# Optimization experiments

Hardware: AMD Instinct MI355X
Metric: run time of the kernel (lower is better)

## Reference

```python
import jax, jax.numpy as jnp
import numpy as np

T, N, F, L, A = 4, 16, 6, 1024, 21  # genomes, tiles, frames, tile length, alphabet
K, U = 20, 256                      # profile width, number of profiles


def setup_inputs() -> dict:
    key = jax.random.key(0)
    k1, k2 = jax.random.split(key)
    X = jax.random.uniform(k1, (T, N, F, L, A), dtype=jnp.float32)
    Q = jnp.ones((A,), dtype=jnp.float32) / A  # uniform background distribution
    # P_logit ~ log(Q) + N(0, 4) as in _getRandomProfiles
    P_logit = (jnp.log(Q)[None, :, None]
               + 4.0 * jax.random.normal(k2, (K, A, U), dtype=jnp.float32))
    return {"X": X, "P_logit": P_logit, "Q": Q}


def reference(X, P_logit, Q):
    # SpecificProfile.call(X) -> (S, R, Z)
    Tb, Nb, Fb, Lb, Ab = X.shape
    k, _, units = P_logit.shape
    # getR: P = softmax(P_logit, axis=1); R = log(max(P / Q, epsilon))
    P = jax.nn.softmax(P_logit, axis=1)                    # [k, A, U]
    epsilon = jnp.mean(Q)                                   # exp(-log(1/mean(Q)))
    R = jnp.log(jnp.maximum(P / Q[None, :, None], epsilon))  # [k, A, U]
    # getZ: conv2d over (length, alphabet) spatial dims, VALID padding
    Xr = X.reshape(Tb * Nb * Fb, Lb, Ab, 1)                 # NHWC
    Kr = R[:, :, None, :]                                   # HWIO: [k, A, 1, U]
    Z = jax.lax.conv_general_dilated(
        Xr, Kr, window_strides=(1, 1), padding='VALID',
        dimension_numbers=('NHWC', 'HWIO', 'NHWC'))          # [TNF, L-k+1, 1, U]
    Z = Z.reshape(Tb, Nb, Fb, Lb - k + 1, units)            # [T, N, F, P, U]
    S = jnp.max(Z, axis=(2, 3))                             # [T, N, U]
    return S, R, Z
```

## Files before the change

### kernel.cpp

```cpp
#include <hip/hip_runtime.h>
#include <hip/hip_bf16.h>
#include <math.h>

#define T_ 4
#define N_ 16
#define F_ 6
#define L_ 1024
#define A_ 21
#define K_ 20
#define U_ 256
#define LOUT 1005
#define NIMG 384
#define SZ_S (T_*N_*U_)
#define SZ_R (K_*A_*U_)

#define XPR 24
#define XROWS 1056
#define NSTEP 15
#define XWCH 7

typedef __attribute__((ext_vector_type(8))) short short8;
typedef __attribute__((ext_vector_type(4))) float f32x4;
typedef __attribute__((ext_vector_type(4))) unsigned int uint4v;

__device__ __forceinline__ unsigned short f2bf(float f) {
  unsigned int u = __float_as_uint(f);
  u += 0x7FFFu + ((u >> 16) & 1u);
  return (unsigned short)(u >> 16);
}

__device__ __forceinline__ void atomicMaxF(float* addr, float val) {
  if (val >= 0.f) atomicMax((int*)addr, __float_as_int(val));
  else            atomicMin((unsigned int*)addr, __float_as_uint(val));
}

__device__ __forceinline__ void gload_lds16(const void* g, void* l) {
  __builtin_amdgcn_global_load_lds(
      (const __attribute__((address_space(1))) void*)g,
      (__attribute__((address_space(3))) void*)l, 16, 0, 0);
}

__global__ void xprep_kernel(const float* __restrict__ X,
                             const float* __restrict__ P_logit,
                             const float* __restrict__ Q,
                             float* __restrict__ out,
                             unsigned short* __restrict__ Rt,
                             unsigned int* __restrict__ Xp32) {
  int t = blockIdx.x * blockDim.x + threadIdx.x;
  if (t < SZ_S) out[t] = -INFINITY;

  if (t < K_ * U_) {
    int k = t / U_;
    int u = t - k * U_;
    const float* pl = P_logit + (size_t)k * A_ * U_ + u;
    float v[A_];
    float m = -INFINITY;
#pragma unroll
    for (int a = 0; a < A_; ++a) { v[a] = pl[(size_t)a * U_]; m = fmaxf(m, v[a]); }
    float s = 0.f;
#pragma unroll
    for (int a = 0; a < A_; ++a) { v[a] = expf(v[a] - m); s += v[a]; }
    float qs = 0.f;
#pragma unroll
    for (int a = 0; a < A_; ++a) qs += Q[a];
    float eps = qs * (1.0f / A_);
    float invs = 1.f / s;
    float* Rout = out + SZ_S;
#pragma unroll
    for (int a = 0; a < XPR; ++a) {
      unsigned short bv = 0;
      if (a < A_) {
        float r = logf(fmaxf(v[a] * invs / Q[a], eps));
        Rout[(size_t)(k * A_ + a) * U_ + u] = r;
        bv = f2bf(r);
      }
      int sl = k * XPR + a;
      Rt[(size_t)(sl >> 5) * (U_ * 32) + u * 32 + (sl & 31)] = bv;
    }
  }

  if (t < NIMG * XROWS * 12) {
    int w  = t % 12;
    int rl = t / 12;
    int row = rl % XROWS;
    int n   = rl / XROWS;
    int c0 = w * 2;
    float v0 = 0.f, v1 = 0.f;
    if (row < L_) {
      const float* xr = X + ((size_t)n * L_ + row) * A_;
      if (c0 < A_)     v0 = xr[c0];
      if (c0 + 1 < A_) v1 = xr[c0 + 1];
    }
    unsigned int o = (unsigned int)f2bf(v0) | ((unsigned int)f2bf(v1) << 16);
    Xp32[(size_t)rl * 12 + w] = o;
  }
}

__global__ __launch_bounds__(256, 1) void conv_kernel(
    const unsigned short* __restrict__ Xp,
    const unsigned short* __restrict__ Rt,
    float* __restrict__ out) {
  __shared__ __align__(16) unsigned short lds_r[NSTEP * 4096];
  __shared__ __align__(16) unsigned short lds_xp[4][XWCH * 512];

  const int n  = blockIdx.z;
  const int u0 = blockIdx.x * 128;
  const int wid  = threadIdx.x >> 6;
  const int lane = threadIdx.x & 63;
  const int wl = wid >> 1;
  const int wu = wid & 1;

  const char* xsrc = (const char*)Xp +
      ((size_t)n * XROWS + wl * 128) * (XPR * 2);
  const char* rsrc = (const char*)Rt + (size_t)u0 * 64;
  char* xdst = (char*)&lds_xp[wid][0];

  for (int c = wid; c < NSTEP * 8; c += 4)
    gload_lds16(rsrc + (size_t)(c >> 3) * (U_ * 64) + (c & 7) * 1024 + lane * 16,
                (char*)lds_r + c * 1024);
#pragma unroll
  for (int c = 0; c < XWCH; ++c)
    gload_lds16(xsrc + c * 1024 + lane * 16, xdst + c * 1024);
  asm volatile("s_waitcnt vmcnt(0)" ::: "memory");
  __builtin_amdgcn_s_barrier();

  const int fl = lane & 15;
  const int fj = lane >> 4;
  const int rfo = (wu * 64 + fl) * 32 + (fj << 3);
  const unsigned short* xb =
      (const unsigned short*)xdst + fl * XPR + (fj << 3);
  const int ug = fj << 2;

  float* Z = out + SZ_S + SZ_R;
  float pmax[4][4];
#pragma unroll
  for (int ut = 0; ut < 4; ++ut)
#pragma unroll
    for (int r = 0; r < 4; ++r) pmax[ut][r] = -INFINITY;

  f32x4 accA[4][8], accB[4][8];
  uint4v xr[XWCH];

#define ZERO(ACC)                                                            \
  {                                                                          \
    _Pragma("unroll")                                                        \
    for (int ut = 0; ut < 4; ++ut)                                           \
      _Pragma("unroll")                                                      \
      for (int lt = 0; lt < 8; ++lt)                                         \
        (ACC)[ut][lt] = (f32x4){0.f, 0.f, 0.f, 0.f};                         \
  }

#define KSTEP(K, ACC)                                                        \
  {                                                                          \
    short8 xfr[8], rfr[4];                                                   \
    const unsigned short* rb = lds_r + (K) * 4096 + rfo;                     \
    _Pragma("unroll")                                                        \
    for (int lt = 0; lt < 8; ++lt)                                           \
      xfr[lt] = *(const short8*)(xb + lt * (16 * XPR) + (K) * 32);           \
    _Pragma("unroll")                                                        \
    for (int ut = 0; ut < 4; ++ut)                                           \
      rfr[ut] = *(const short8*)(rb + ut * (16 * 32));                       \
    _Pragma("unroll")                                                        \
    for (int ut = 0; ut < 4; ++ut)                                           \
      _Pragma("unroll")                                                      \
      for (int lt = 0; lt < 8; ++lt)                                         \
        (ACC)[ut][lt] = __builtin_amdgcn_mfma_f32_16x16x32_bf16(             \
            rfr[ut], xfr[lt], (ACC)[ut][lt], 0, 0, 0);                       \
  }

#define STORE4(ACC, TT, LT)                                                  \
  {                                                                          \
    const int l = (TT) * 256 + wl * 128 + (LT) * 16 + fl;                    \
    float* zrow = Z + ((size_t)n * LOUT + l) * U_ + u0 + wu * 64 + ug;       \
    _Pragma("unroll")                                                        \
    for (int ut = 0; ut < 4; ++ut) {                                         \
      f32x4 v = (ACC)[ut][LT];                                               \
      *(f32x4*)(zrow + ut * 16) = v;                                         \
      _Pragma("unroll")                                                      \
      for (int r = 0; r < 4; ++r) pmax[ut][r] = fmaxf(pmax[ut][r], v[r]);    \
    }                                                                        \
  }

#define XLOADS(T1)                                                           \
  {                                                                          \
    const char* xs = xsrc + (size_t)(T1) * (256 * XPR * 2);                  \
    _Pragma("unroll")                                                        \
    for (int c = 0; c < XWCH; ++c)                                           \
      xr[c] = *(const uint4v*)(xs + c * 1024 + lane * 16);                   \
  }

#define XWRITE()                                                             \
  {                                                                          \
    _Pragma("unroll")                                                        \
    for (int c = 0; c < XWCH; ++c)                                           \
      *(uint4v*)(xdst + c * 1024 + lane * 16) = xr[c];                       \
  }

  ZERO(accA)
  XLOADS(1)
#pragma unroll
  for (int k = 0; k < NSTEP; ++k) KSTEP(k, accA)
  asm volatile("s_waitcnt vmcnt(0)" ::: "memory");
  XWRITE()

  ZERO(accB)
  XLOADS(2)
#pragma unroll
  for (int k = 0; k < NSTEP; ++k) {
    KSTEP(k, accB)
    if (k >= 1 && k <= 8) STORE4(accA, 0, k - 1)
  }
  asm volatile("s_waitcnt vmcnt(32)" ::: "memory");
  XWRITE()

  ZERO(accA)
  XLOADS(3)
#pragma unroll
  for (int k = 0; k < NSTEP; ++k) {
    KSTEP(k, accA)
    if (k >= 1 && k <= 8) STORE4(accB, 1, k - 1)
  }
  asm volatile("s_waitcnt vmcnt(32)" ::: "memory");
  XWRITE()

  ZERO(accB)
#pragma unroll
  for (int k = 0; k < NSTEP; ++k) {
    KSTEP(k, accB)
    if (k >= 1 && k <= 8) STORE4(accA, 2, k - 1)
  }

#pragma unroll
  for (int lt = 0; lt < 8; ++lt) {
    const int l = 768 + wl * 128 + lt * 16 + fl;
    if (l < LOUT) {
      float* zrow = Z + ((size_t)n * LOUT + l) * U_ + u0 + wu * 64 + ug;
#pragma unroll
      for (int ut = 0; ut < 4; ++ut) {
        f32x4 v = accB[ut][lt];
        *(f32x4*)(zrow + ut * 16) = v;
#pragma unroll
        for (int r = 0; r < 4; ++r) pmax[ut][r] = fmaxf(pmax[ut][r], v[r]);
      }
    }
  }

#undef ZERO
#undef KSTEP
#undef STORE4
#undef XLOADS
#undef XWRITE

#pragma unroll
  for (int off = 1; off < 16; off <<= 1)
#pragma unroll
    for (int ut = 0; ut < 4; ++ut)
#pragma unroll
      for (int r = 0; r < 4; ++r)
        pmax[ut][r] = fmaxf(pmax[ut][r], __shfl_xor(pmax[ut][r], off));

  if (fl == 0) {
    const int tn = n / F_;
    float* Sp = out + (size_t)tn * U_ + u0 + wu * 64 + ug;
#pragma unroll
    for (int ut = 0; ut < 4; ++ut)
#pragma unroll
      for (int r = 0; r < 4; ++r)
        atomicMaxF(Sp + ut * 16 + r, pmax[ut][r]);
  }
}

extern "C" void kernel_launch(void* const* d_in, const int* in_sizes, int n_in,
                              void* d_out, int out_size, void* d_ws, size_t ws_size,
                              hipStream_t stream) {
  const float* X       = (const float*)d_in[0];
  const float* P_logit = (const float*)d_in[1];
  const float* Q       = (const float*)d_in[2];
  float* out = (float*)d_out;

  unsigned short* Rt = (unsigned short*)d_ws;
  unsigned short* Xp = (unsigned short*)((char*)d_ws + 262144);

  int xthreads = NIMG * XROWS * 12;
  hipLaunchKernelGGL(xprep_kernel, dim3((xthreads + 255) / 256), dim3(256),
                     0, stream, X, P_logit, Q, out, Rt, (unsigned int*)Xp);
  dim3 grid(2, 1, NIMG);
  hipLaunchKernelGGL(conv_kernel, grid, dim3(256), 0, stream, Xp, Rt, out);
}
```

Baseline: 130.9 us.

## Make conv kernel persistent over three images with cross-image store pipelining

The grid shrinks from 768 to 256 blocks, and each block now handles three images in sequence (n0, n0+128, n0+256). The R tile is loaded into LDS once per block instead of once per image. The next image's first X chunk is prefetched during the previous image's last tile. The previous image's final, partly valid tile is stored while the next image's first tile is computed, and stores are spread over selected k-steps. Invalid tail rows are redirected to a dump buffer in workspace to avoid branches, which assumes the workspace has room for it. Fewer blocks on a large GPU may reduce parallelism and load balance.

```diff
diff --git a/kernel.cpp b/kernel.cpp
--- a/kernel.cpp
+++ b/kernel.cpp
@@ -99,28 +99,31 @@
 __global__ __launch_bounds__(256, 1) void conv_kernel(
     const unsigned short* __restrict__ Xp,
     const unsigned short* __restrict__ Rt,
-    float* __restrict__ out) {
+    float* __restrict__ out,
+    float* __restrict__ dump) {
   __shared__ __align__(16) unsigned short lds_r[NSTEP * 4096];
   __shared__ __align__(16) unsigned short lds_xp[4][XWCH * 512];
 
-  const int n  = blockIdx.z;
+  const int n0 = blockIdx.z;
   const int u0 = blockIdx.x * 128;
   const int wid  = threadIdx.x >> 6;
   const int lane = threadIdx.x & 63;
   const int wl = wid >> 1;
   const int wu = wid & 1;
 
-  const char* xsrc = (const char*)Xp +
-      ((size_t)n * XROWS + wl * 128) * (XPR * 2);
   const char* rsrc = (const char*)Rt + (size_t)u0 * 64;
   char* xdst = (char*)&lds_xp[wid][0];
 
   for (int c = wid; c < NSTEP * 8; c += 4)
     gload_lds16(rsrc + (size_t)(c >> 3) * (U_ * 64) + (c & 7) * 1024 + lane * 16,
                 (char*)lds_r + c * 1024);
-#pragma unroll
-  for (int c = 0; c < XWCH; ++c)
-    gload_lds16(xsrc + c * 1024 + lane * 16, xdst + c * 1024);
+  {
+    const char* xs = (const char*)Xp +
+        ((size_t)n0 * XROWS + wl * 128) * (XPR * 2);
+#pragma unroll
+    for (int c = 0; c < XWCH; ++c)
+      gload_lds16(xs + c * 1024 + lane * 16, xdst + c * 1024);
+  }
   asm volatile("s_waitcnt vmcnt(0)" ::: "memory");
   __builtin_amdgcn_s_barrier();
 
@@ -141,6 +144,9 @@
   f32x4 accA[4][8], accB[4][8];
   uint4v xr[XWCH];
 
+#define SGK(k) ((k)==1?0:(k)==2?1:(k)==4?2:(k)==5?3:(k)==7?4:(k)==9?5:   \
+                (k)==10?6:(k)==12?7:-1)
+
 #define ZERO(ACC)                                                            \
   {                                                                          \
     _Pragma("unroll")                                                        \
@@ -168,10 +174,10 @@
             rfr[ut], xfr[lt], (ACC)[ut][lt], 0, 0, 0);                       \
   }
 
-#define STORE4(ACC, TT, LT)                                                  \
+#define STORE4(ACC, NN, TT, LT)                                              \
   {                                                                          \
     const int l = (TT) * 256 + wl * 128 + (LT) * 16 + fl;                    \
-    float* zrow = Z + ((size_t)n * LOUT + l) * U_ + u0 + wu * 64 + ug;       \
+    float* zrow = Z + ((size_t)(NN) * LOUT + l) * U_ + u0 + wu * 64 + ug;    \
     _Pragma("unroll")                                                        \
     for (int ut = 0; ut < 4; ++ut) {                                         \
       f32x4 v = (ACC)[ut][LT];                                               \
@@ -181,9 +187,26 @@
     }                                                                        \
   }
 
-#define XLOADS(T1)                                                           \
-  {                                                                          \
-    const char* xs = xsrc + (size_t)(T1) * (256 * XPR * 2);                  \
+#define STORE4C(ACC, NN, LT)                                                 \
+  {                                                                          \
+    const int l = 768 + wl * 128 + (LT) * 16 + fl;                           \
+    const bool valid = (l < LOUT);                                           \
+    float* zreal = Z + ((size_t)(NN) * LOUT + l) * U_ + u0 + wu * 64 + ug;   \
+    float* zrow = valid ? zreal : (dump + lane * 4);                         \
+    _Pragma("unroll")                                                        \
+    for (int ut = 0; ut < 4; ++ut) {                                         \
+      f32x4 v = (ACC)[ut][LT];                                               \
+      *(f32x4*)(zrow + ut * 16) = v;                                         \
+      _Pragma("unroll")                                                      \
+      for (int r = 0; r < 4; ++r)                                            \
+        pmax[ut][r] = valid ? fmaxf(pmax[ut][r], v[r]) : pmax[ut][r];        \
+    }                                                                        \
+  }
+
+#define XLOADS(NN, TT)                                                       \
+  {                                                                          \
+    const char* xs = (const char*)Xp +                                       \
+        (((size_t)(NN) * XROWS + (TT) * 256 + wl * 128)) * (XPR * 2);        \
     _Pragma("unroll")                                                        \
     for (int c = 0; c < XWCH; ++c)                                           \
       xr[c] = *(const uint4v*)(xs + c * 1024 + lane * 16);                   \
@@ -196,45 +219,83 @@
       *(uint4v*)(xdst + c * 1024 + lane * 16) = xr[c];                       \
   }
 
-  ZERO(accA)
-  XLOADS(1)
-#pragma unroll
-  for (int k = 0; k < NSTEP; ++k) KSTEP(k, accA)
-  asm volatile("s_waitcnt vmcnt(0)" ::: "memory");
-  XWRITE()
-
-  ZERO(accB)
-  XLOADS(2)
-#pragma unroll
-  for (int k = 0; k < NSTEP; ++k) {
-    KSTEP(k, accB)
-    if (k >= 1 && k <= 8) STORE4(accA, 0, k - 1)
-  }
-  asm volatile("s_waitcnt vmcnt(32)" ::: "memory");
-  XWRITE()
-
-  ZERO(accA)
-  XLOADS(3)
-#pragma unroll
-  for (int k = 0; k < NSTEP; ++k) {
-    KSTEP(k, accA)
-    if (k >= 1 && k <= 8) STORE4(accB, 1, k - 1)
-  }
-  asm volatile("s_waitcnt vmcnt(32)" ::: "memory");
-  XWRITE()
-
-  ZERO(accB)
-#pragma unroll
-  for (int k = 0; k < NSTEP; ++k) {
-    KSTEP(k, accB)
-    if (k >= 1 && k <= 8) STORE4(accA, 2, k - 1)
+#define FLUSH(NN)                                                            \
+  {                                                                          \
+    _Pragma("unroll")                                                        \
+    for (int off = 1; off < 16; off <<= 1)                                   \
+      _Pragma("unroll")                                                      \
+      for (int ut = 0; ut < 4; ++ut)                                         \
+        _Pragma("unroll")                                                    \
+        for (int r = 0; r < 4; ++r)                                          \
+          pmax[ut][r] = fmaxf(pmax[ut][r], __shfl_xor(pmax[ut][r], off));    \
+    if (fl == 0) {                                                           \
+      float* Sp = out + (size_t)((NN) / F_) * U_ + u0 + wu * 64 + ug;        \
+      _Pragma("unroll")                                                      \
+      for (int ut = 0; ut < 4; ++ut)                                         \
+        _Pragma("unroll")                                                    \
+        for (int r = 0; r < 4; ++r)                                          \
+          atomicMaxF(Sp + ut * 16 + r, pmax[ut][r]);                         \
+    }                                                                        \
+    _Pragma("unroll")                                                        \
+    for (int ut = 0; ut < 4; ++ut)                                           \
+      _Pragma("unroll")                                                      \
+      for (int r = 0; r < 4; ++r) pmax[ut][r] = -INFINITY;                   \
+  }
+
+#pragma unroll 1
+  for (int j = 0; j < 3; ++j) {
+    const int n = n0 + (j << 7);
+
+    ZERO(accA)
+    XLOADS(n, 1)
+#pragma unroll
+    for (int k = 0; k < NSTEP; ++k) {
+      KSTEP(k, accA)
+      if (j > 0 && SGK(k) >= 0) STORE4C(accB, n - 128, SGK(k))
+    }
+    if (j == 0) asm volatile("s_waitcnt vmcnt(0)" ::: "memory");
+    else        asm volatile("s_waitcnt vmcnt(32)" ::: "memory");
+    XWRITE()
+    if (j > 0) FLUSH(n - 128)
+
+    ZERO(accB)
+    XLOADS(n, 2)
+#pragma unroll
+    for (int k = 0; k < NSTEP; ++k) {
+      KSTEP(k, accB)
+      if (SGK(k) >= 0) STORE4(accA, n, 0, SGK(k))
+    }
+    asm volatile("s_waitcnt vmcnt(32)" ::: "memory");
+    XWRITE()
+
+    ZERO(accA)
+    XLOADS(n, 3)
+#pragma unroll
+    for (int k = 0; k < NSTEP; ++k) {
+      KSTEP(k, accA)
+      if (SGK(k) >= 0) STORE4(accB, n, 1, SGK(k))
+    }
+    asm volatile("s_waitcnt vmcnt(32)" ::: "memory");
+    XWRITE()
+
+    ZERO(accB)
+    if (j < 2) XLOADS(n + 128, 0)
+#pragma unroll
+    for (int k = 0; k < NSTEP; ++k) {
+      KSTEP(k, accB)
+      if (SGK(k) >= 0) STORE4(accA, n, 2, SGK(k))
+    }
+    if (j < 2) {
+      asm volatile("s_waitcnt vmcnt(32)" ::: "memory");
+      XWRITE()
+    }
   }
 
 #pragma unroll
   for (int lt = 0; lt < 8; ++lt) {
     const int l = 768 + wl * 128 + lt * 16 + fl;
     if (l < LOUT) {
-      float* zrow = Z + ((size_t)n * LOUT + l) * U_ + u0 + wu * 64 + ug;
+      float* zrow = Z + ((size_t)(n0 + 256) * LOUT + l) * U_ + u0 + wu * 64 + ug;
 #pragma unroll
       for (int ut = 0; ut < 4; ++ut) {
         f32x4 v = accB[ut][lt];
@@ -244,30 +305,16 @@
       }
     }
   }
-
+  FLUSH(n0 + 256)
+
+#undef SGK
 #undef ZERO
 #undef KSTEP
 #undef STORE4
+#undef STORE4C
 #undef XLOADS
 #undef XWRITE
-
-#pragma unroll
-  for (int off = 1; off < 16; off <<= 1)
-#pragma unroll
-    for (int ut = 0; ut < 4; ++ut)
-#pragma unroll
-      for (int r = 0; r < 4; ++r)
-        pmax[ut][r] = fmaxf(pmax[ut][r], __shfl_xor(pmax[ut][r], off));
-
-  if (fl == 0) {
-    const int tn = n / F_;
-    float* Sp = out + (size_t)tn * U_ + u0 + wu * 64 + ug;
-#pragma unroll
-    for (int ut = 0; ut < 4; ++ut)
-#pragma unroll
-      for (int r = 0; r < 4; ++r)
-        atomicMaxF(Sp + ut * 16 + r, pmax[ut][r]);
-  }
+#undef FLUSH
 }
 
 extern "C" void kernel_launch(void* const* d_in, const int* in_sizes, int n_in,
@@ -280,10 +327,13 @@
 
   unsigned short* Rt = (unsigned short*)d_ws;
   unsigned short* Xp = (unsigned short*)((char*)d_ws + 262144);
+  const size_t xp_bytes = (size_t)NIMG * XROWS * XPR * 2;
+  float* dump = (float*)((char*)d_ws + 262144 + xp_bytes);
 
   int xthreads = NIMG * XROWS * 12;
   hipLaunchKernelGGL(xprep_kernel, dim3((xthreads + 255) / 256), dim3(256),
                      0, stream, X, P_logit, Q, out, Rt, (unsigned int*)Xp);
-  dim3 grid(2, 1, NIMG);
-  hipLaunchKernelGGL(conv_kernel, grid, dim3(256), 0, stream, Xp, Rt, out);
-}
+  dim3 grid(2, 1, 128);
+  hipLaunchKernelGGL(conv_kernel, grid, dim3(256), 0, stream,
+                     Xp, Rt, out, dump);
+}
```

After: 247.5 us. 89.0% more time.
